# Performance work log

Hardware: AMD Instinct MI355X
Metric: run time of the kernel (lower is better)

The kernel has to match this reference:

```python
import jax, jax.numpy as jnp
import numpy as np

BATCH = 256
VOCAB = 50000
NUM_TOPICS = 50
TIME_SLICES = 10
EMBED_DIM = 1024


def setup_inputs() -> dict:
    key = jax.random.key(0)
    k1, k2, k3, k4 = jax.random.split(key, 4)
    theta = jax.random.uniform(k1, (BATCH, NUM_TOPICS), dtype=jnp.float32)
    theta = theta / jnp.sum(theta, axis=-1, keepdims=True)  # topic distribution
    word_embeddings = jax.random.normal(k2, (VOCAB, EMBED_DIM), dtype=jnp.float32)
    topic_embeddings = jax.random.normal(k3, (TIME_SLICES, NUM_TOPICS, EMBED_DIM), dtype=jnp.float32)
    time_index = jax.random.randint(k4, (BATCH,), 0, TIME_SLICES, dtype=jnp.int64)
    return {"theta": theta, "word_embeddings": word_embeddings,
            "topic_embeddings": topic_embeddings, "time_index": time_index}


def reference(theta, word_embeddings, topic_embeddings, time_index):
    # beta_t = softmax(topic_embeddings[t] @ W^T) over vocab, for all time slices: (T, K, V)
    logits = jnp.einsum('tke,ve->tkv', topic_embeddings, word_embeddings)
    betas = jax.nn.softmax(logits, axis=-1)
    # word_dist[i] = theta[i] @ betas[time_index[i]]. Compute for all t then gather
    # (avoids materializing a (B, K, V) gathered tensor).
    all_out = jnp.einsum('bk,tkv->btv', theta, betas)  # (B, T, V)
    out = jnp.take_along_axis(all_out, time_index[:, None, None], axis=1)[:, 0, :]
    return out  # (B, V)
```

## Files before the change

### kernel.cpp

```cpp
#include <hip/hip_runtime.h>
#include <hip/hip_bf16.h>


typedef __bf16 bf16_t;
typedef __bf16 bf16x4 __attribute__((ext_vector_type(4)));
typedef __bf16 bf16x8 __attribute__((ext_vector_type(8)));
typedef float f32x4 __attribute__((ext_vector_type(4)));

typedef __attribute__((address_space(1))) void gvoid;
typedef __attribute__((address_space(3))) void svoid;
#define GLDS(SRC, DST) \
    __builtin_amdgcn_global_load_lds((gvoid*)(SRC), (svoid*)(DST), 16, 0, 0)
#define MFMA16(A, B, C) __builtin_amdgcn_mfma_f32_16x16x32_bf16((A), (B), (C), 0, 0, 0)

#define SHIFT 180.0f
#define TTS 40

__device__ __forceinline__ void cvt8(float4 a, float4 b, bf16x8& h, bf16x8& l)
{
    float f[8] = {a.x, a.y, a.z, a.w, b.x, b.y, b.z, b.w};
#pragma unroll
    for (int j = 0; j < 8; ++j) {
        bf16_t hh = (bf16_t)f[j];
        h[j] = hh;
        l[j] = (bf16_t)(f[j] - (float)hh);
    }
}

__global__ void prep(const float* __restrict__ x, bf16_t* __restrict__ hi,
                     bf16_t* __restrict__ lo, float* __restrict__ rsum)
{
    int i = blockIdx.x * 256 + threadIdx.x;
    if (i < 512) rsum[i] = 0.f;
    if (i < 512000) {
        float v = x[i];
        bf16_t h = (bf16_t)v;
        hi[i] = h;
        lo[i] = (bf16_t)(v - (float)h);
    }
}

__global__ __launch_bounds__(256, 3)
void gemm_logits(const bf16_t* __restrict__ Ahi, const bf16_t* __restrict__ Alo,
                 const float* __restrict__ W, bf16_t* __restrict__ Pt,
                 float* __restrict__ Rsum)
{
    __shared__ __align__(16) bf16_t sm[24576];
    bf16_t* AsH = sm;
    bf16_t* AsL = sm + 8192;
    bf16_t* BsH = sm + 16384;
    bf16_t* BsL = sm + 20480;

    const int tid = threadIdx.x;
    const int wv = tid >> 6, lane = tid & 63;
    const int bm0 = blockIdx.x * 128;
    const int bn0 = blockIdx.y * 64;
    const int lrow = lane & 15, q = lane >> 4;
    const int srow = lane >> 3, sgrp = (lane & 7) ^ srow;

    const int wrow_l = tid >> 2;
    int wrow_g = bn0 + wrow_l; if (wrow_g > 49999) wrow_g = 49999;
    const int kq = tid & 3;
    const float4* wp = (const float4*)(W + (long)wrow_g * 1024 + kq * 16);
    const int kga = kq * 2;
    const int so_a = wrow_l * 64 + ((kga ^ (wrow_l & 7)) * 8);
    const int so_b = wrow_l * 64 + (((kga + 1) ^ (wrow_l & 7)) * 8);

    f32x4 acc[2][4] = {};

    float4 wcur[4], wnxt[4];
#pragma unroll
    for (int j = 0; j < 4; ++j) wcur[j] = wp[j];

    for (int k0 = 0; k0 < 1024; k0 += 64) {
#pragma unroll
        for (int cc = 0; cc < 4; ++cc) {
            const int ch = wv * 4 + cc;
            int ar = bm0 + ch * 8 + srow; if (ar > 499) ar = 499;
            GLDS(Ahi + (long)ar * 1024 + k0 + sgrp * 8, AsH + ch * 512);
            GLDS(Alo + (long)ar * 1024 + k0 + sgrp * 8, AsL + ch * 512);
        }
        if (k0 < 960) {
            const int o = (k0 + 64) >> 2;
#pragma unroll
            for (int j = 0; j < 4; ++j) wnxt[j] = wp[o + j];
        }
        {
            bf16x8 h0, l0, h1, l1;
            cvt8(wcur[0], wcur[1], h0, l0);
            cvt8(wcur[2], wcur[3], h1, l1);
            *(bf16x8*)(BsH + so_a) = h0;
            *(bf16x8*)(BsL + so_a) = l0;
            *(bf16x8*)(BsH + so_b) = h1;
            *(bf16x8*)(BsL + so_b) = l1;
        }
        __syncthreads();
#pragma unroll
        for (int kk = 0; kk < 2; ++kk) {
            const int kg = kk * 4 + q;
            bf16x8 ah[2], al[2], bh[4], bl[4];
#pragma unroll
            for (int a = 0; a < 2; ++a) {
                const int row = wv * 32 + a * 16 + lrow;
                const int off = row * 64 + ((kg ^ (row & 7)) * 8);
                ah[a] = *(const bf16x8*)(AsH + off);
                al[a] = *(const bf16x8*)(AsL + off);
            }
#pragma unroll
            for (int b = 0; b < 4; ++b) {
                const int n = b * 16 + lrow;
                const int off = n * 64 + ((kg ^ (n & 7)) * 8);
                bh[b] = *(const bf16x8*)(BsH + off);
                bl[b] = *(const bf16x8*)(BsL + off);
            }
#pragma unroll
            for (int a = 0; a < 2; ++a)
#pragma unroll
                for (int b = 0; b < 4; ++b) {
                    acc[a][b] = MFMA16(ah[a], bh[b], acc[a][b]);
                    acc[a][b] = MFMA16(ah[a], bl[b], acc[a][b]);
                    acc[a][b] = MFMA16(al[a], bh[b], acc[a][b]);
                }
        }
        __syncthreads();
#pragma unroll
        for (int j = 0; j < 4; ++j) wcur[j] = wnxt[j];
    }

#pragma unroll
    for (int a = 0; a < 2; ++a) {
        float rs[4] = {0.f, 0.f, 0.f, 0.f};
#pragma unroll
        for (int b = 0; b < 4; ++b) {
            const bool cok = (bn0 + b * 16 + lrow) < 50000;
#pragma unroll
            for (int r = 0; r < 4; ++r) {
                const float e = __expf(acc[a][b][r] - SHIFT);
                acc[a][b][r] = e;
                if (cok) rs[r] += e;
            }
        }
#pragma unroll
        for (int r = 0; r < 4; ++r) {
            float v = rs[r];
            v += __shfl_xor(v, 1, 16);
            v += __shfl_xor(v, 2, 16);
            v += __shfl_xor(v, 4, 16);
            v += __shfl_xor(v, 8, 16);
            const int row = bm0 + wv * 32 + a * 16 + q * 4 + r;
            if (lrow == 0 && row < 500) atomicAdd(Rsum + row, v);
        }
    }
    bf16_t* Tt = sm + wv * (64 * TTS);
#pragma unroll
    for (int a = 0; a < 2; ++a)
#pragma unroll
        for (int b = 0; b < 4; ++b) {
            bf16x4 p;
#pragma unroll
            for (int r = 0; r < 4; ++r) p[r] = (bf16_t)acc[a][b][r];
            *(bf16x4*)(Tt + (b * 16 + lrow) * TTS + a * 16 + q * 4) = p;
        }
    const long kbase = bm0 + wv * 32;
#pragma unroll
    for (int it = 0; it < 4; ++it) {
        const int u = it * 64 + lane;
        const int vl = u >> 2, ck = u & 3;
        bf16x8 d = *(const bf16x8*)(Tt + vl * TTS + ck * 8);
        *(bf16x8*)(Pt + (long)(bn0 + vl) * 512 + kbase + ck * 8) = d;
    }
}

__global__ void build_theta2(const float* __restrict__ theta,
                             const int* __restrict__ tidx,
                             const float* __restrict__ rsum,
                             bf16_t* __restrict__ T2)
{
    const int i = blockIdx.x, r = threadIdx.x;
    const int base = tidx[i] * 50;
    bf16_t v = (bf16_t)0.0f;
    if (r >= base && r < base + 50)
        v = (bf16_t)(theta[i * 50 + (r - base)] / rsum[r]);
    T2[i * 512 + r] = v;
}

__global__ __launch_bounds__(256, 4)
void gemm_out(const bf16_t* __restrict__ T2, const bf16_t* __restrict__ Pt,
              float* __restrict__ out)
{
    __shared__ __align__(16) bf16_t As[256 * 64];
    __shared__ __align__(16) bf16_t Bs[64 * 64];
    const int tid = threadIdx.x;
    const int wave = tid >> 6, lane = tid & 63;
    const int bn0 = blockIdx.x * 64;
    const int lrow = lane & 15, q = lane >> 4;
    const int srow = lane >> 3, sgrp = (lane & 7) ^ srow;

    f32x4 acc[4][4] = {};

    for (int k0 = 0; k0 < 512; k0 += 64) {
#pragma unroll
        for (int cc = 0; cc < 8; ++cc) {
            const int ch = wave * 8 + cc;
            GLDS(T2 + (ch * 8 + srow) * 512 + k0 + sgrp * 8, As + ch * 512);
        }
#pragma unroll
        for (int cc = 0; cc < 2; ++cc) {
            const int ch = wave * 2 + cc;
            const long brow = bn0 + ch * 8 + srow;
            GLDS(Pt + brow * 512 + k0 + sgrp * 8, Bs + ch * 512);
        }
        __syncthreads();
#pragma unroll
        for (int kk = 0; kk < 2; ++kk) {
            const int kg = kk * 4 + q;
            bf16x8 af[4], bfr[4];
#pragma unroll
            for (int a = 0; a < 4; ++a) {
                const int row = wave * 64 + a * 16 + lrow;
                af[a] = *(const bf16x8*)(As + row * 64 + ((kg ^ (row & 7)) * 8));
            }
#pragma unroll
            for (int b = 0; b < 4; ++b) {
                const int n = b * 16 + lrow;
                bfr[b] = *(const bf16x8*)(Bs + n * 64 + ((kg ^ (n & 7)) * 8));
            }
#pragma unroll
            for (int a = 0; a < 4; ++a)
#pragma unroll
                for (int b = 0; b < 4; ++b)
                    acc[a][b] = MFMA16(af[a], bfr[b], acc[a][b]);
        }
        __syncthreads();
    }
#pragma unroll
    for (int a = 0; a < 4; ++a) {
        const int row0 = wave * 64 + a * 16 + q * 4;
#pragma unroll
        for (int b = 0; b < 4; ++b) {
            const int col = bn0 + b * 16 + lrow;
            if (col < 50000) {
#pragma unroll
                for (int r = 0; r < 4; ++r)
                    out[(long)(row0 + r) * 50000 + col] = acc[a][b][r];
            }
        }
    }
}

extern "C" void kernel_launch(void* const* d_in, const int* in_sizes, int n_in,
                              void* d_out, int out_size, void* d_ws, size_t ws_size,
                              hipStream_t stream)
{
    const float* theta = (const float*)d_in[0];
    const float* wemb  = (const float*)d_in[1];
    const float* temb  = (const float*)d_in[2];
    const int*   tidx  = (const int*)d_in[3];
    float* out = (float*)d_out;

    char* ws = (char*)d_ws;
    bf16_t* Pt    = (bf16_t*)ws;
    float*  rsum  = (float*)(ws + 51249152);
    bf16_t* a_hi  = (bf16_t*)(ws + 51251200);
    bf16_t* a_lo  = (bf16_t*)(ws + 52275200);
    bf16_t* T2    = (bf16_t*)(ws + 53299200);

    prep        <<<dim3(2000),   256, 0, stream>>>(temb, a_hi, a_lo, rsum);
    gemm_logits <<<dim3(4, 782), 256, 0, stream>>>(a_hi, a_lo, wemb, Pt, rsum);
    build_theta2<<<dim3(256),    512, 0, stream>>>(theta, tidx, rsum, T2);
    gemm_out    <<<dim3(782),    256, 0, stream>>>(T2, Pt, out);
}
```

Before: 466.7 us.

## Double-buffer logits GEMM with 512-thread 128x128 tiles and XCD-aware block mapping

The logits GEMM grows to 8 waves per block, each block covering a 128x128 tile, so every W row loaded and split into hi/lo is reused across twice as many columns. Shared memory becomes a double buffer: the next k-slice of A is issued via global_load_lds and the next W slice is converted while MFMAs run on the current one, which leaves one barrier per iteration. The 1D grid is remapped so blocks dispatched to the same XCD work on neighbouring vocab tiles, and s_setprio raises priority around the MFMA bursts. The cost is 128KB of LDS per block and fewer resident blocks, which reduces occupancy.

```diff
diff --git a/kernel.cpp b/kernel.cpp
--- a/kernel.cpp
+++ b/kernel.cpp
@@ -40,21 +40,23 @@
     }
 }
 
-__global__ __launch_bounds__(256, 3)
+__global__ __launch_bounds__(512, 2)
 void gemm_logits(const bf16_t* __restrict__ Ahi, const bf16_t* __restrict__ Alo,
                  const float* __restrict__ W, bf16_t* __restrict__ Pt,
                  float* __restrict__ Rsum)
 {
-    __shared__ __align__(16) bf16_t sm[24576];
-    bf16_t* AsH = sm;
-    bf16_t* AsL = sm + 8192;
-    bf16_t* BsH = sm + 16384;
-    bf16_t* BsL = sm + 20480;
+    __shared__ __align__(16) bf16_t sm[65536];
 
     const int tid = threadIdx.x;
     const int wv = tid >> 6, lane = tid & 63;
-    const int bm0 = blockIdx.x * 128;
-    const int bn0 = blockIdx.y * 64;
+    const int wm = wv >> 1, wn = wv & 1;
+
+    const int lin = blockIdx.x;
+    const int xcd = lin & 7, wi = lin >> 3;
+    const int nid = (xcd < 4 ? xcd * 196 : 784 + (xcd - 4) * 195) + wi;
+    const int bm0 = (nid & 3) * 128;
+    const int bn0 = (nid >> 2) * 128;
+
     const int lrow = lane & 15, q = lane >> 4;
     const int srow = lane >> 3, sgrp = (lane & 7) ^ srow;
 
@@ -67,52 +69,70 @@
     const int so_b = wrow_l * 64 + (((kga + 1) ^ (wrow_l & 7)) * 8);
 
     f32x4 acc[2][4] = {};
-
-    float4 wcur[4], wnxt[4];
-#pragma unroll
-    for (int j = 0; j < 4; ++j) wcur[j] = wp[j];
-
-    for (int k0 = 0; k0 < 1024; k0 += 64) {
-#pragma unroll
-        for (int cc = 0; cc < 4; ++cc) {
-            const int ch = wv * 4 + cc;
-            int ar = bm0 + ch * 8 + srow; if (ar > 499) ar = 499;
-            GLDS(Ahi + (long)ar * 1024 + k0 + sgrp * 8, AsH + ch * 512);
-            GLDS(Alo + (long)ar * 1024 + k0 + sgrp * 8, AsL + ch * 512);
-        }
-        if (k0 < 960) {
-            const int o = (k0 + 64) >> 2;
-#pragma unroll
-            for (int j = 0; j < 4; ++j) wnxt[j] = wp[o + j];
-        }
-        {
-            bf16x8 h0, l0, h1, l1;
-            cvt8(wcur[0], wcur[1], h0, l0);
-            cvt8(wcur[2], wcur[3], h1, l1);
-            *(bf16x8*)(BsH + so_a) = h0;
-            *(bf16x8*)(BsL + so_a) = l0;
-            *(bf16x8*)(BsH + so_b) = h1;
-            *(bf16x8*)(BsL + so_b) = l1;
-        }
-        __syncthreads();
+    float4 wnx[4];
+
+#pragma unroll
+    for (int j = 0; j < 4; ++j) wnx[j] = wp[j];
+#pragma unroll
+    for (int cc = 0; cc < 2; ++cc) {
+        const int ch = wv * 2 + cc;
+        int ar = bm0 + ch * 8 + srow; if (ar > 499) ar = 499;
+        GLDS(Ahi + (long)ar * 1024 + sgrp * 8, sm + ch * 512);
+        GLDS(Alo + (long)ar * 1024 + sgrp * 8, sm + 8192 + ch * 512);
+    }
+    {
+        bf16x8 h0, l0, h1, l1;
+        cvt8(wnx[0], wnx[1], h0, l0);
+        cvt8(wnx[2], wnx[3], h1, l1);
+        *(bf16x8*)(sm + 16384 + so_a) = h0;
+        *(bf16x8*)(sm + 24576 + so_a) = l0;
+        *(bf16x8*)(sm + 16384 + so_b) = h1;
+        *(bf16x8*)(sm + 24576 + so_b) = l1;
+    }
+    __syncthreads();
+
+    for (int t = 0; t < 16; ++t) {
+        const int cb = t & 1, nb = cb ^ 1;
+        bf16_t* AsH = sm + cb * 32768;
+        bf16_t* AsL = AsH + 8192;
+        bf16_t* BsH = AsH + 16384;
+        bf16_t* BsL = AsH + 24576;
+
+        if (t < 15) {
+            const int o = (t + 1) * 16;
+#pragma unroll
+            for (int j = 0; j < 4; ++j) wnx[j] = wp[o + j];
+            bf16_t* nAsH = sm + nb * 32768;
+            bf16_t* nAsL = nAsH + 8192;
+            const int k0n = (t + 1) * 64;
+#pragma unroll
+            for (int cc = 0; cc < 2; ++cc) {
+                const int ch = wv * 2 + cc;
+                int ar = bm0 + ch * 8 + srow; if (ar > 499) ar = 499;
+                GLDS(Ahi + (long)ar * 1024 + k0n + sgrp * 8, nAsH + ch * 512);
+                GLDS(Alo + (long)ar * 1024 + k0n + sgrp * 8, nAsL + ch * 512);
+            }
+        }
+
 #pragma unroll
         for (int kk = 0; kk < 2; ++kk) {
             const int kg = kk * 4 + q;
             bf16x8 ah[2], al[2], bh[4], bl[4];
 #pragma unroll
             for (int a = 0; a < 2; ++a) {
-                const int row = wv * 32 + a * 16 + lrow;
+                const int row = wm * 32 + a * 16 + lrow;
                 const int off = row * 64 + ((kg ^ (row & 7)) * 8);
                 ah[a] = *(const bf16x8*)(AsH + off);
                 al[a] = *(const bf16x8*)(AsL + off);
             }
 #pragma unroll
             for (int b = 0; b < 4; ++b) {
-                const int n = b * 16 + lrow;
+                const int n = wn * 64 + b * 16 + lrow;
                 const int off = n * 64 + ((kg ^ (n & 7)) * 8);
                 bh[b] = *(const bf16x8*)(BsH + off);
                 bl[b] = *(const bf16x8*)(BsL + off);
             }
+            __builtin_amdgcn_s_setprio(1);
 #pragma unroll
             for (int a = 0; a < 2; ++a)
 #pragma unroll
@@ -121,10 +141,21 @@
                     acc[a][b] = MFMA16(ah[a], bl[b], acc[a][b]);
                     acc[a][b] = MFMA16(al[a], bh[b], acc[a][b]);
                 }
+            __builtin_amdgcn_s_setprio(0);
+        }
+
+        if (t < 15) {
+            bf16_t* nBsH = sm + nb * 32768 + 16384;
+            bf16_t* nBsL = nBsH + 8192;
+            bf16x8 h0, l0, h1, l1;
+            cvt8(wnx[0], wnx[1], h0, l0);
+            cvt8(wnx[2], wnx[3], h1, l1);
+            *(bf16x8*)(nBsH + so_a) = h0;
+            *(bf16x8*)(nBsL + so_a) = l0;
+            *(bf16x8*)(nBsH + so_b) = h1;
+            *(bf16x8*)(nBsL + so_b) = l1;
         }
         __syncthreads();
-#pragma unroll
-        for (int j = 0; j < 4; ++j) wcur[j] = wnxt[j];
     }
 
 #pragma unroll
@@ -132,7 +163,7 @@
         float rs[4] = {0.f, 0.f, 0.f, 0.f};
 #pragma unroll
         for (int b = 0; b < 4; ++b) {
-            const bool cok = (bn0 + b * 16 + lrow) < 50000;
+            const bool cok = (bn0 + wn * 64 + b * 16 + lrow) < 50000;
 #pragma unroll
             for (int r = 0; r < 4; ++r) {
                 const float e = __expf(acc[a][b][r] - SHIFT);
@@ -147,7 +178,7 @@
             v += __shfl_xor(v, 2, 16);
             v += __shfl_xor(v, 4, 16);
             v += __shfl_xor(v, 8, 16);
-            const int row = bm0 + wv * 32 + a * 16 + q * 4 + r;
+            const int row = bm0 + wm * 32 + a * 16 + q * 4 + r;
             if (lrow == 0 && row < 500) atomicAdd(Rsum + row, v);
         }
     }
@@ -161,13 +192,14 @@
             for (int r = 0; r < 4; ++r) p[r] = (bf16_t)acc[a][b][r];
             *(bf16x4*)(Tt + (b * 16 + lrow) * TTS + a * 16 + q * 4) = p;
         }
-    const long kbase = bm0 + wv * 32;
+    const long kbase = bm0 + wm * 32;
+    const int cbase = bn0 + wn * 64;
 #pragma unroll
     for (int it = 0; it < 4; ++it) {
         const int u = it * 64 + lane;
         const int vl = u >> 2, ck = u & 3;
         bf16x8 d = *(const bf16x8*)(Tt + vl * TTS + ck * 8);
-        *(bf16x8*)(Pt + (long)(bn0 + vl) * 512 + kbase + ck * 8) = d;
+        *(bf16x8*)(Pt + (long)(cbase + vl) * 512 + kbase + ck * 8) = d;
     }
 }
 
@@ -265,8 +297,8 @@
     bf16_t* a_lo  = (bf16_t*)(ws + 52275200);
     bf16_t* T2    = (bf16_t*)(ws + 53299200);
 
-    prep        <<<dim3(2000),   256, 0, stream>>>(temb, a_hi, a_lo, rsum);
-    gemm_logits <<<dim3(4, 782), 256, 0, stream>>>(a_hi, a_lo, wemb, Pt, rsum);
-    build_theta2<<<dim3(256),    512, 0, stream>>>(theta, tidx, rsum, T2);
-    gemm_out    <<<dim3(782),    256, 0, stream>>>(T2, Pt, out);
-}
+    prep        <<<dim3(2000), 256, 0, stream>>>(temb, a_hi, a_lo, rsum);
+    gemm_logits <<<dim3(1564), 512, 0, stream>>>(a_hi, a_lo, wemb, Pt, rsum);
+    build_theta2<<<dim3(256),  512, 0, stream>>>(theta, tidx, rsum, T2);
+    gemm_out    <<<dim3(782),  256, 0, stream>>>(T2, Pt, out);
+}
```

New measurement: 501.9 us. +7.6%, slower.

## Enlarge logits GEMM tile to 128x128 with XCD-aware block remapping

Applied to the files above, without the earlier changes.

Grows the gemm_logits block tile from 128x64 to 128x128, using a 2x2 wave grid where each wave computes 64x64 (4x4 MFMA tiles). This doubles the reuse of A/B data staged in LDS. Blocks are remapped to a 1D grid so that the four M-tiles sharing a W slice land on the same XCD, which should improve L2 reuse of the word embeddings. The W prefetch is moved after the barrier, and s_setprio is set around the MFMA loop. In exchange, the larger register and LDS footprint cuts occupancy from 3 to 2 blocks per CU.

```diff
diff --git a/kernel.cpp b/kernel.cpp
--- a/kernel.cpp
+++ b/kernel.cpp
@@ -14,7 +14,7 @@
 #define MFMA16(A, B, C) __builtin_amdgcn_mfma_f32_16x16x32_bf16((A), (B), (C), 0, 0, 0)
 
 #define SHIFT 180.0f
-#define TTS 40
+#define TTS2 72
 
 __device__ __forceinline__ void cvt8(float4 a, float4 b, bf16x8& h, bf16x8& l)
 {
@@ -40,39 +40,46 @@
     }
 }
 
-__global__ __launch_bounds__(256, 3)
+__global__ __launch_bounds__(256, 2)
 void gemm_logits(const bf16_t* __restrict__ Ahi, const bf16_t* __restrict__ Alo,
                  const float* __restrict__ W, bf16_t* __restrict__ Pt,
                  float* __restrict__ Rsum)
 {
-    __shared__ __align__(16) bf16_t sm[24576];
+    __shared__ __align__(16) bf16_t sm[32768];
     bf16_t* AsH = sm;
     bf16_t* AsL = sm + 8192;
     bf16_t* BsH = sm + 16384;
-    bf16_t* BsL = sm + 20480;
+    bf16_t* BsL = sm + 24576;
 
     const int tid = threadIdx.x;
     const int wv = tid >> 6, lane = tid & 63;
-    const int bm0 = blockIdx.x * 128;
-    const int bn0 = blockIdx.y * 64;
+    const int wm = wv >> 1, wn = wv & 1;
+
+    const int lin = blockIdx.x;
+    const int xcd = lin & 7, wi = lin >> 3;
+    const int nid = (xcd < 4 ? xcd * 196 : 784 + (xcd - 4) * 195) + wi;
+    const int bm0 = (nid & 3) * 128;
+    const int bn0 = (nid >> 2) * 128;
+
     const int lrow = lane & 15, q = lane >> 4;
     const int srow = lane >> 3, sgrp = (lane & 7) ^ srow;
 
-    const int wrow_l = tid >> 2;
+    const int wrow_l = tid >> 1;
     int wrow_g = bn0 + wrow_l; if (wrow_g > 49999) wrow_g = 49999;
-    const int kq = tid & 3;
-    const float4* wp = (const float4*)(W + (long)wrow_g * 1024 + kq * 16);
-    const int kga = kq * 2;
-    const int so_a = wrow_l * 64 + ((kga ^ (wrow_l & 7)) * 8);
-    const int so_b = wrow_l * 64 + (((kga + 1) ^ (wrow_l & 7)) * 8);
-
-    f32x4 acc[2][4] = {};
-
-    float4 wcur[4], wnxt[4];
-#pragma unroll
-    for (int j = 0; j < 4; ++j) wcur[j] = wp[j];
-
-    for (int k0 = 0; k0 < 1024; k0 += 64) {
+    const int kq = tid & 1;
+    const float4* wp = (const float4*)(W + (long)wrow_g * 1024) + kq * 8;
+    int so[4];
+#pragma unroll
+    for (int jj = 0; jj < 4; ++jj)
+        so[jj] = wrow_l * 64 + (((kq * 4 + jj) ^ (wrow_l & 7)) * 8);
+
+    f32x4 acc[4][4] = {};
+    float4 wcur[8], wnxt[8];
+#pragma unroll
+    for (int j = 0; j < 8; ++j) wcur[j] = wp[j];
+
+    for (int t = 0; t < 16; ++t) {
+        const int k0 = t * 64;
 #pragma unroll
         for (int cc = 0; cc < 4; ++cc) {
             const int ch = wv * 4 + cc;
@@ -80,59 +87,61 @@
             GLDS(Ahi + (long)ar * 1024 + k0 + sgrp * 8, AsH + ch * 512);
             GLDS(Alo + (long)ar * 1024 + k0 + sgrp * 8, AsL + ch * 512);
         }
-        if (k0 < 960) {
-            const int o = (k0 + 64) >> 2;
-#pragma unroll
-            for (int j = 0; j < 4; ++j) wnxt[j] = wp[o + j];
-        }
-        {
-            bf16x8 h0, l0, h1, l1;
-            cvt8(wcur[0], wcur[1], h0, l0);
-            cvt8(wcur[2], wcur[3], h1, l1);
-            *(bf16x8*)(BsH + so_a) = h0;
-            *(bf16x8*)(BsL + so_a) = l0;
-            *(bf16x8*)(BsH + so_b) = h1;
-            *(bf16x8*)(BsL + so_b) = l1;
-        }
-        __syncthreads();
+#pragma unroll
+        for (int jj = 0; jj < 4; ++jj) {
+            bf16x8 h, l;
+            cvt8(wcur[2 * jj], wcur[2 * jj + 1], h, l);
+            *(bf16x8*)(BsH + so[jj]) = h;
+            *(bf16x8*)(BsL + so[jj]) = l;
+        }
+        __syncthreads();
+        if (t < 15) {
+            const int o = (t + 1) * 16;
+#pragma unroll
+            for (int j = 0; j < 8; ++j) wnxt[j] = wp[o + j];
+        }
 #pragma unroll
         for (int kk = 0; kk < 2; ++kk) {
             const int kg = kk * 4 + q;
-            bf16x8 ah[2], al[2], bh[4], bl[4];
-#pragma unroll
-            for (int a = 0; a < 2; ++a) {
-                const int row = wv * 32 + a * 16 + lrow;
+            bf16x8 ah[4], al[4], bh[4], bl[4];
+#pragma unroll
+            for (int a = 0; a < 4; ++a) {
+                const int row = wm * 64 + a * 16 + lrow;
                 const int off = row * 64 + ((kg ^ (row & 7)) * 8);
                 ah[a] = *(const bf16x8*)(AsH + off);
                 al[a] = *(const bf16x8*)(AsL + off);
             }
 #pragma unroll
             for (int b = 0; b < 4; ++b) {
-                const int n = b * 16 + lrow;
+                const int n = wn * 64 + b * 16 + lrow;
                 const int off = n * 64 + ((kg ^ (n & 7)) * 8);
                 bh[b] = *(const bf16x8*)(BsH + off);
                 bl[b] = *(const bf16x8*)(BsL + off);
             }
-#pragma unroll
-            for (int a = 0; a < 2; ++a)
+            __builtin_amdgcn_s_setprio(1);
+#pragma unroll
+            for (int a = 0; a < 4; ++a)
 #pragma unroll
                 for (int b = 0; b < 4; ++b) {
                     acc[a][b] = MFMA16(ah[a], bh[b], acc[a][b]);
                     acc[a][b] = MFMA16(ah[a], bl[b], acc[a][b]);
                     acc[a][b] = MFMA16(al[a], bh[b], acc[a][b]);
                 }
-        }
-        __syncthreads();
-#pragma unroll
-        for (int j = 0; j < 4; ++j) wcur[j] = wnxt[j];
-    }
-
-#pragma unroll
-    for (int a = 0; a < 2; ++a) {
+            __builtin_amdgcn_s_setprio(0);
+        }
+        __syncthreads();
+        if (t < 15) {
+#pragma unroll
+            for (int j = 0; j < 8; ++j) wcur[j] = wnxt[j];
+        }
+    }
+
+#pragma unroll
+    for (int a = 0; a < 4; ++a) {
         float rs[4] = {0.f, 0.f, 0.f, 0.f};
 #pragma unroll
         for (int b = 0; b < 4; ++b) {
-            const bool cok = (bn0 + b * 16 + lrow) < 50000;
+            const bool cok = (bn0 + wn * 64 + b * 16 + lrow) < 50000;
 #pragma unroll
             for (int r = 0; r < 4; ++r) {
                 const float e = __expf(acc[a][b][r] - SHIFT);
@@ -147,27 +156,28 @@
             v += __shfl_xor(v, 2, 16);
             v += __shfl_xor(v, 4, 16);
             v += __shfl_xor(v, 8, 16);
-            const int row = bm0 + wv * 32 + a * 16 + q * 4 + r;
+            const int row = bm0 + wm * 64 + a * 16 + q * 4 + r;
             if (lrow == 0 && row < 500) atomicAdd(Rsum + row, v);
         }
     }
-    bf16_t* Tt = sm + wv * (64 * TTS);
-#pragma unroll
-    for (int a = 0; a < 2; ++a)
+    bf16_t* Tt = sm + wv * (64 * TTS2);
+#pragma unroll
+    for (int a = 0; a < 4; ++a)
 #pragma unroll
         for (int b = 0; b < 4; ++b) {
             bf16x4 p;
 #pragma unroll
             for (int r = 0; r < 4; ++r) p[r] = (bf16_t)acc[a][b][r];
-            *(bf16x4*)(Tt + (b * 16 + lrow) * TTS + a * 16 + q * 4) = p;
-        }
-    const long kbase = bm0 + wv * 32;
-#pragma unroll
-    for (int it = 0; it < 4; ++it) {
+            *(bf16x4*)(Tt + (b * 16 + lrow) * TTS2 + a * 16 + q * 4) = p;
+        }
+    const long kbase = bm0 + wm * 64;
+    const int cbase = bn0 + wn * 64;
+#pragma unroll
+    for (int it = 0; it < 8; ++it) {
         const int u = it * 64 + lane;
-        const int vl = u >> 2, ck = u & 3;
-        bf16x8 d = *(const bf16x8*)(Tt + vl * TTS + ck * 8);
-        *(bf16x8*)(Pt + (long)(bn0 + vl) * 512 + kbase + ck * 8) = d;
+        const int vl = u >> 3, ck = u & 7;
+        bf16x8 d = *(const bf16x8*)(Tt + vl * TTS2 + ck * 8);
+        *(bf16x8*)(Pt + (long)(cbase + vl) * 512 + kbase + ck * 8) = d;
     }
 }
 
@@ -265,8 +275,8 @@
     bf16_t* a_lo  = (bf16_t*)(ws + 52275200);
     bf16_t* T2    = (bf16_t*)(ws + 53299200);
 
-    prep        <<<dim3(2000),   256, 0, stream>>>(temb, a_hi, a_lo, rsum);
-    gemm_logits <<<dim3(4, 782), 256, 0, stream>>>(a_hi, a_lo, wemb, Pt, rsum);
-    build_theta2<<<dim3(256),    512, 0, stream>>>(theta, tidx, rsum, T2);
-    gemm_out    <<<dim3(782),    256, 0, stream>>>(T2, Pt, out);
-}
+    prep        <<<dim3(2000), 256, 0, stream>>>(temb, a_hi, a_lo, rsum);
+    gemm_logits <<<dim3(1564), 256, 0, stream>>>(a_hi, a_lo, wemb, Pt, rsum);
+    build_theta2<<<dim3(256),  512, 0, stream>>>(theta, tidx, rsum, T2);
+    gemm_out    <<<dim3(782),  256, 0, stream>>>(T2, Pt, out);
+}
```

Measured after the change: 464.6 us. No clear change (-0.4%).
